# Performance work log

Measured on AMD Instinct MI355X. Metric: run time of the kernel, lower is better.

Reference implementation:

```python
import jax, jax.numpy as jnp
import numpy as np

B, NQ, NK, D, H = 4, 1025, 1024, 1024, 16
C = D // H          # per-head channels = 64
DFF = 1024          # FFN hidden, hard-coded in source
LN_EPS = 1e-5


def setup_inputs() -> dict:
    key = jax.random.key(0)
    ks = jax.random.split(key, 12)
    s = 0.02
    return {
        "q": jax.random.normal(ks[0], (B, NQ, D), jnp.float32),
        "k": jax.random.normal(ks[1], (B, NK, D), jnp.float32),
        "v": jax.random.normal(ks[2], (B, NK, D), jnp.float32),
        "w_qk": jax.random.normal(ks[3], (D, D), jnp.float32) * s,
        "dummy": jax.random.normal(ks[4], (1, D), jnp.float32),
        "w1": jax.random.normal(ks[5], (C, C // 2), jnp.float32) * s,
        "b1": jnp.zeros((C // 2,), jnp.float32),
        "w2": jax.random.normal(ks[6], (C, C // 2), jnp.float32) * s,
        "b2": jnp.zeros((C // 2,), jnp.float32),
        "w3": jax.random.normal(ks[7], (2 * C, C), jnp.float32) * s,
        "b3": jnp.zeros((C,), jnp.float32),
        "fw1": jax.random.normal(ks[8], (C, DFF), jnp.float32) * s,
        "fb1": jnp.zeros((DFF,), jnp.float32),
        "fw2": jax.random.normal(ks[9], (DFF, C), jnp.float32) * s,
        "fb2": jnp.zeros((C,), jnp.float32),
        "ln_g": jnp.ones((C,), jnp.float32),
        "ln_b": jnp.zeros((C,), jnp.float32),
    }


def _split_heads(x):
    # 'b n (h c) -> (b h) n c'
    b, n, _ = x.shape
    return x.reshape(b, n, H, C).transpose(0, 2, 1, 3).reshape(b * H, n, C)


def _l2norm(x):
    n = jnp.linalg.norm(x, axis=-1, keepdims=True)
    return x / jnp.maximum(n, 1e-12)


def reference(q, k, v, w_qk, dummy, w1, b1, w2, b2, w3, b3,
              fw1, fb1, fw2, fb2, ln_g, ln_b):
    b, nq, d = q.shape
    residual = q
    qp = q @ w_qk
    kp = jnp.concatenate(
        [k @ w_qk, jnp.broadcast_to(dummy[None], (b, 1, d))], axis=1)
    vp = jnp.concatenate([v, jnp.zeros((b, 1, d), v.dtype)], axis=1)

    qh, kh, vh, rh = map(_split_heads, (qp, kp, vp, residual))

    # cosine-similarity attention, ReLU instead of softmax (dropout p=0)
    attn = jnp.einsum('bic,bjc->bij', _l2norm(qh), _l2norm(kh))
    attn = jax.nn.relu(attn)
    out = jnp.einsum('bij,bjc->bic', attn, vh)  # (b*h, nq, c)

    o1 = jax.nn.relu((out * rh) @ w1 + b1)
    o2 = jax.nn.relu((rh - out) @ w2 + b2)
    o = jnp.concatenate([o1, o2, rh], axis=-1) @ w3 + b3

    # FFN with residual + LayerNorm (dropouts are identity at p=0)
    t = o + rh
    t = t + (jax.nn.relu(t @ fw1 + fb1) @ fw2 + fb2)
    mu = jnp.mean(t, axis=-1, keepdims=True)
    var = jnp.mean(jnp.square(t - mu), axis=-1, keepdims=True)
    t = (t - mu) / jnp.sqrt(var + LN_EPS) * ln_g + ln_b

    t = t + vh  # requires nq == nk + 1

    # '(b h) n c -> b n (h c)'
    return t.reshape(b, H, nq, C).transpose(0, 2, 1, 3).reshape(b, nq, d)
```

## Files before the change

kernel.cpp:

```cpp
#include <hip/hip_runtime.h>
#include <hip/hip_bf16.h>

#define DEV __device__ __forceinline__

typedef __attribute__((ext_vector_type(4))) float  f32x4;
typedef __attribute__((ext_vector_type(8))) short  s16x8;
typedef __attribute__((ext_vector_type(8))) __bf16 bf16x8;

#define NQ   1025
#define BH   64
#define NPAD 1152
#define MT   65600
#define DFF  1024

DEV short f2bf(float f){
  unsigned u = __builtin_bit_cast(unsigned, f);
  u = u + 0x7fffu + ((u >> 16) & 1u);
  return (short)(u >> 16);
}
DEV float bf2f(short s){
  unsigned u = ((unsigned)(unsigned short)s) << 16;
  return __builtin_bit_cast(float, u);
}
DEV f32x4 zero4(){ f32x4 z; z[0]=0.f; z[1]=0.f; z[2]=0.f; z[3]=0.f; return z; }
DEV s16x8 zero8(){ s16x8 z; for(int e=0;e<8;e++) z[e]=0; return z; }

DEV f32x4 mfma16(s16x8 a, s16x8 b, f32x4 c){
  return __builtin_amdgcn_mfma_f32_16x16x32_bf16(
      __builtin_bit_cast(bf16x8, a), __builtin_bit_cast(bf16x8, b), c, 0, 0, 0);
}

DEV void gll16(const void* g, void* l){
  __builtin_amdgcn_global_load_lds((const __attribute__((address_space(1))) void*)g,
                                   (__attribute__((address_space(3))) void*)l, 16, 0, 0);
}

DEV s16x8 lds_frag(const char* base, int row, int k8){
  int byte = row*128 + k8*2; byte ^= (row & 7) << 4;
  return *(const s16x8*)(base + byte);
}
DEV void lds_write16(char* base, int row, int k8, s16x8 v){
  int byte = row*128 + k8*2; byte ^= (row & 7) << 4;
  *(s16x8*)(base + byte) = v;
}
DEV void lds_write2(char* base, int row, int col, short v){
  int byte = row*128 + col*2; byte ^= (row & 7) << 4;
  *(short*)(base + byte) = v;
}
DEV void lds_w16_256(char* base, int row, int col, s16x8 v){
  int byte = row*256 + col*2; byte ^= (row & 7) << 4;
  *(s16x8*)(base + byte) = v;
}
DEV s16x8 lds_r16_256(const char* base, int row, int col){
  int byte = row*256 + col*2; byte ^= (row & 7) << 4;
  return *(const s16x8*)(base + byte);
}
DEV void lds_w2_256(char* base, int row, int col, short v){
  int byte = row*256 + col*2; byte ^= (row & 7) << 4;
  *(short*)(base + byte) = v;
}
DEV void blob_w16(char* blob, int row, int k8, s16x8 v){
  int byte = row*128 + k8*2; byte ^= (row & 7) << 4;
  *(s16x8*)(blob + byte) = v;
}

__global__ void k_tcvt(const float* __restrict__ in, int irs, int rin,
                       short* __restrict__ out, int ors){
  __shared__ float tile[32][33];
  int r0 = blockIdx.x*32, c0 = blockIdx.y*32;
  int tx = threadIdx.x, ty = threadIdx.y;
  for (int i=ty;i<32;i+=8){
    int r = r0+i;
    tile[i][tx] = (r < rin) ? in[(long)r*irs + c0 + tx] : 0.f;
  }
  __syncthreads();
  for (int i=ty;i<32;i+=8)
    out[(long)(c0+i)*ors + r0 + tx] = f2bf(tile[tx][i]);
}

__global__ __launch_bounds__(256)
void k_cvtA(const float* __restrict__ q, const float* __restrict__ kk, char* __restrict__ ab){
  int mt = blockIdx.x, kt = blockIdx.y;
  int tid = threadIdx.x;
  int r = tid>>1, ks = (tid&1)*32;
  int pr = mt*128 + r;
  int part = pr >= 4608;
  int pp = part ? pr-4608 : pr;
  int b = pp/NPAD, i = pp%NPAD;
  const float* src = nullptr;
  if (!part && i < 1025) src = q  + ((long)(b*1025+i))*1024 + kt*64 + ks;
  if ( part && i < 1024) src = kk + ((long)(b*1024+i))*1024 + kt*64 + ks;
  char* blob = ab + ((long)(mt*16+kt))*16384;
  #pragma unroll
  for (int c8=0;c8<32;c8+=8){
    s16x8 vv = zero8();
    if (src){
      f32x4 f0 = *(const f32x4*)(src + c8);
      f32x4 f1 = *(const f32x4*)(src + c8 + 4);
      #pragma unroll
      for(int e=0;e<4;e++){ vv[e]=f2bf(f0[e]); vv[4+e]=f2bf(f1[e]); }
    }
    blob_w16(blob, r, ks+c8, vv);
  }
}

__global__ __launch_bounds__(256)
void k_cvtW(const float* __restrict__ w, char* __restrict__ wb){
  __shared__ float T[64][129];
  int nt = blockIdx.x, kt = blockIdx.y;
  int tid = threadIdx.x;
  for (int idx=tid; idx<8192; idx+=256){
    int kr = idx>>7, nc = idx&127;
    T[kr][nc] = w[(long)(kt*64+kr)*1024 + nt*128+nc];
  }
  __syncthreads();
  int r = tid>>1, ks=(tid&1)*32;
  char* blob = wb + ((long)(nt*16+kt))*16384;
  #pragma unroll
  for (int c8=0;c8<32;c8+=8){
    s16x8 vv;
    #pragma unroll
    for(int e=0;e<8;e++) vv[e] = f2bf(T[ks+c8+e][r]);
    blob_w16(blob, r, ks+c8, vv);
  }
}

__global__ __launch_bounds__(256)
void k_cvtV(const float* __restrict__ v, char* __restrict__ vb){
  __shared__ float T[64][65];
  int jt = blockIdx.x, bh = blockIdx.y;
  int b = bh>>4, h = bh&15;
  int tid=threadIdx.x;
  for (int idx=tid; idx<4096; idx+=256){
    int jr = idx>>6, cc = idx&63;
    int j = jt*64+jr;
    T[jr][cc] = (j<1024)? v[((long)(b*1024+j))*1024 + h*64+cc] : 0.f;
  }
  __syncthreads();
  int r = tid>>2, js=(tid&3)*16;
  char* blob = vb + ((long)(bh*18+jt))*8192;
  #pragma unroll
  for (int c8=0;c8<16;c8+=8){
    s16x8 vv;
    #pragma unroll
    for(int e=0;e<8;e++) vv[e] = f2bf(T[js+c8+e][r]);
    blob_w16(blob, r, js+c8, vv);
  }
}

__global__ __launch_bounds__(256,2)
void k_proj(const char* __restrict__ ab, const char* __restrict__ wb,
            char* __restrict__ qpB, char* __restrict__ kpB,
            float* __restrict__ qnorm, float* __restrict__ knorm){
  __shared__ char SM[32768];
  char* A = SM; char* Bm = SM+16384;
  int flat = blockIdx.x;
  int g = (flat&7)*72 + (flat>>3);
  int mt = g>>3, nt = g&7;
  int tid=threadIdx.x, lane=tid&63, wv=tid>>6, lr=lane&15, lg=lane>>4;
  f32x4 acc[4][4];
  for(int a=0;a<4;a++) for(int b=0;b<4;b++) acc[a][b]=zero4();
  int wm=(wv>>1)*64, wn=(wv&1)*64;
  for (int kt=0; kt<16; kt++){
    const char* asrc = ab + ((long)(mt*16+kt))*16384 + wv*4096 + lane*16;
    const char* bsrc = wb + ((long)(nt*16+kt))*16384 + wv*4096 + lane*16;
    char* adst = A + wv*4096;  char* bdst = Bm + wv*4096;
    #pragma unroll
    for (int t=0;t<4;t++){
      gll16(asrc + t*1024, adst + t*1024);
      gll16(bsrc + t*1024, bdst + t*1024);
    }
    __syncthreads();
    #pragma unroll
    for (int kc=0;kc<64;kc+=32){
      int lk = kc + (lg<<3);
      s16x8 af[4], bfr[4];
      #pragma unroll
      for(int i=0;i<4;i++) af[i]  = lds_frag(A,  wm + i*16 + lr, lk);
      #pragma unroll
      for(int i=0;i<4;i++) bfr[i] = lds_frag(Bm, wn + i*16 + lr, lk);
      #pragma unroll
      for(int mi=0;mi<4;mi++)
        #pragma unroll
        for(int ni=0;ni<4;ni++) acc[mi][ni] = mfma16(af[mi], bfr[ni], acc[mi][ni]);
    }
    __syncthreads();
  }
  int head = nt*2 + (wv&1);
  #pragma unroll
  for(int mi=0;mi<4;mi++)
  #pragma unroll
  for(int j=0;j<4;j++){
    float ss = 0.f;
    #pragma unroll
    for(int ni=0;ni<4;ni++){ float x=acc[mi][ni][j]; ss += x*x; }
    ss += __shfl_xor(ss,1); ss += __shfl_xor(ss,2);
    ss += __shfl_xor(ss,4); ss += __shfl_xor(ss,8);
    if (lr==0){
      int pr = mt*128 + wm + mi*16 + lg*4 + j;
      int part = pr>=4608; int pp = part? pr-4608:pr;
      int b = pp/NPAD, i = pp%NPAD;
      float scv = 1.f/fmaxf(sqrtf(ss), 1e-12f);
      (part? knorm : qnorm)[(b*16+head)*NPAD + i] = scv;
    }
  }
  #pragma unroll
  for(int mi=0;mi<4;mi++)
  #pragma unroll
  for(int ni=0;ni<4;ni++)
  #pragma unroll
  for(int j=0;j<4;j++)
    lds_w2_256(SM, wm+mi*16+lg*4+j, wn+ni*16+lr, f2bf(acc[mi][ni][j]));
  __syncthreads();
  {
    int r = tid>>1, half = tid&1;
    int pr = mt*128 + r;
    int part = pr>=4608; int pp = part? pr-4608:pr;
    int b = pp/NPAD, i = pp%NPAD;
    int h2 = nt*2 + half;
    char* dst = (part? kpB : qpB) + ((long)((b*16+h2)*18 + (i>>6)))*8192;
    int rr = i&63;
    #pragma unroll
    for (int c8=0;c8<64;c8+=8){
      s16x8 vv = lds_r16_256(SM, r, half*64 + c8);
      blob_w16(dst, rr, c8, vv);
    }
  }
}

__global__ __launch_bounds__(256,2)
void k_attn(const char* __restrict__ qpB, const char* __restrict__ kpB,
            const char* __restrict__ vtB,
            const float* __restrict__ qnorm, const float* __restrict__ knorm,
            short* __restrict__ att){
  __shared__ char SM[49152];
  char* Q = SM; char* KT = SM+16384; char* VT = KT+8192; char* P = VT+8192;
  int flat = blockIdx.x;
  int g = (flat&7)*72 + (flat>>3);
  int bh = g/9, it = g%9;
  int i0 = it*128;
  int tid=threadIdx.x, lane=tid&63, wv=tid>>6, lr=lane&15, lg=lane>>4;
  {
    const char* src = qpB + ((long)(bh*18 + it*2))*8192 + wv*4096 + lane*16;
    char* dst = Q + wv*4096;
    #pragma unroll
    for (int t=0;t<4;t++) gll16(src + t*1024, dst + t*1024);
  }
  float rq[2][4];
  #pragma unroll
  for(int mi=0;mi<2;mi++)
  #pragma unroll
  for(int j=0;j<4;j++)
    rq[mi][j] = qnorm[bh*NPAD + i0 + wv*32+mi*16+lg*4+j];
  f32x4 oacc[2][4];
  for(int a=0;a<2;a++) for(int b=0;b<4;b++) oacc[a][b]=zero4();
  for (int jt=0; jt<18; ++jt){
    {
      const char* ks = kpB + ((long)(bh*18+jt))*8192 + wv*2048 + lane*16;
      const char* vs = vtB + ((long)(bh*18+jt))*8192 + wv*2048 + lane*16;
      gll16(ks,      KT + wv*2048);
      gll16(ks+1024, KT + wv*2048 + 1024);
      gll16(vs,      VT + wv*2048);
      gll16(vs+1024, VT + wv*2048 + 1024);
    }
    float rk[4];
    #pragma unroll
    for(int ni=0;ni<4;ni++) rk[ni] = knorm[bh*NPAD + jt*64 + ni*16+lr];
    __syncthreads();
    f32x4 sc[2][4];
    for(int a=0;a<2;a++) for(int b=0;b<4;b++) sc[a][b]=zero4();
    #pragma unroll
    for(int kc=0;kc<64;kc+=32){
      int lk = kc + (lg<<3);
      s16x8 af[2], bfr[4];
      #pragma unroll
      for(int i=0;i<2;i++) af[i]=lds_frag(Q, wv*32 + i*16 + lr, lk);
      #pragma unroll
      for(int i=0;i<4;i++) bfr[i]=lds_frag(KT, i*16 + lr, lk);
      #pragma unroll
      for(int mi=0;mi<2;mi++)
        #pragma unroll
        for(int ni=0;ni<4;ni++) sc[mi][ni]=mfma16(af[mi],bfr[ni],sc[mi][ni]);
    }
    #pragma unroll
    for(int mi=0;mi<2;mi++)
    #pragma unroll
    for(int ni=0;ni<4;ni++)
    #pragma unroll
    for(int j=0;j<4;j++){
      float x = sc[mi][ni][j] * rq[mi][j] * rk[ni];
      x = x>0.f?x:0.f;
      lds_write2(P, wv*32 + mi*16 + lg*4 + j, ni*16 + lr, f2bf(x));
    }
    __syncthreads();
    #pragma unroll
    for(int kc=0;kc<64;kc+=32){
      int lk = kc + (lg<<3);
      s16x8 pf[2], vf[4];
      #pragma unroll
      for(int i=0;i<2;i++) pf[i]=lds_frag(P, wv*32 + i*16 + lr, lk);
      #pragma unroll
      for(int i=0;i<4;i++) vf[i]=lds_frag(VT, i*16 + lr, lk);
      #pragma unroll
      for(int mi=0;mi<2;mi++)
        #pragma unroll
        for(int ni=0;ni<4;ni++) oacc[mi][ni]=mfma16(pf[mi],vf[ni],oacc[mi][ni]);
    }
    __syncthreads();
  }
  char* OS = SM+16384;
  #pragma unroll
  for(int mi=0;mi<2;mi++)
  #pragma unroll
  for(int ni=0;ni<4;ni++)
  #pragma unroll
  for(int j=0;j<4;j++)
    lds_write2(OS, wv*32+mi*16+lg*4+j, ni*16+lr, f2bf(oacc[mi][ni][j]));
  __syncthreads();
  {
    int r = tid>>1, half = tid&1;
    int i = i0 + r;
    if (i < 1025){
      short* dst = att + ((long)bh*1025 + i)*64 + half*32;
      #pragma unroll
      for (int u=0; u<32; u+=8){
        s16x8 vv = lds_frag(OS, r, half*32 + u);
        *(s16x8*)(dst + u) = vv;
      }
    }
  }
}

__global__ __launch_bounds__(256,1)
void k_tailpre(const short* __restrict__ att, const float* __restrict__ q,
    const float* __restrict__ w1, const float* __restrict__ b1,
    const float* __restrict__ w2, const float* __restrict__ b2,
    const float* __restrict__ w3, const float* __restrict__ b3,
    float* __restrict__ tf){
  __shared__ char X   [128*128*2];
  __shared__ char Y   [128*128*2];
  __shared__ char WbdT[ 64*128*2];
  __shared__ char W3T [ 64*128*2];
  long m0 = (long)blockIdx.x*128;
  int tid=threadIdx.x, lane=tid&63, wv=tid>>6, lr=lane&15, lg=lane>>4;
  for (int idx=tid; idx<64*128; idx+=256){
    int n = idx>>7, kx = idx&127;
    float wb = (n<32) ? (kx<64 ? w1[kx*32+n] : 0.f)
                      : (kx>=64 ? w2[(kx-64)*32+(n-32)] : 0.f);
    lds_w2_256(WbdT, n, kx, f2bf(wb));
    lds_w2_256(W3T,  n, kx, f2bf(w3[kx*64+n]));
  }
  {
    int r = tid>>1, ks=(tid&1)*32;
    long m = m0 + r;
    if (m < MT){
      int bh = (int)(m/1025); int i=(int)(m-(long)bh*1025); int b=bh>>4, h=bh&15;
      const short* asrc = att + m*64 + ks;
      const float* qsrc = q + ((long)b*1025 + i)*1024 + h*64 + ks;
      #pragma unroll
      for (int c8=0;c8<32;c8+=8){
        s16x8 av = *(const s16x8*)(asrc + c8);
        f32x4 q0 = *(const f32x4*)(qsrc + c8);
        f32x4 q1 = *(const f32x4*)(qsrc + c8 + 4);
        s16x8 x1v, x2v, rhv;
        #pragma unroll
        for(int e=0;e<4;e++){
          float o0=bf2f(av[e]),   r0=q0[e];
          float o1=bf2f(av[4+e]), r1=q1[e];
          x1v[e]=f2bf(o0*r0);   x1v[4+e]=f2bf(o1*r1);
          x2v[e]=f2bf(r0-o0);   x2v[4+e]=f2bf(r1-o1);
          rhv[e]=f2bf(r0);      rhv[4+e]=f2bf(r1);
        }
        lds_w16_256(X, r, ks+c8,    x1v);
        lds_w16_256(X, r, 64+ks+c8, x2v);
        lds_w16_256(Y, r, 64+ks+c8, rhv);
      }
    } else {
      s16x8 z = zero8();
      #pragma unroll
      for (int c8=0;c8<32;c8+=8){
        lds_w16_256(X, r, ks+c8, z);
        lds_w16_256(X, r, 64+ks+c8, z);
        lds_w16_256(Y, r, 64+ks+c8, z);
      }
    }
  }
  __syncthreads();
  f32x4 a1[2][4];
  for(int a=0;a<2;a++) for(int b=0;b<4;b++) a1[a][b]=zero4();
  #pragma unroll
  for (int kc=0;kc<128;kc+=32){
    int lk = kc + (lg<<3);
    s16x8 af[2], bfr[4];
    #pragma unroll
    for(int i=0;i<2;i++) af[i]=lds_r16_256(X, wv*32+i*16+lr, lk);
    #pragma unroll
    for(int i=0;i<4;i++) bfr[i]=lds_r16_256(WbdT, i*16+lr, lk);
    #pragma unroll
    for(int mi=0;mi<2;mi++)
      #pragma unroll
      for(int ni=0;ni<4;ni++) a1[mi][ni]=mfma16(af[mi],bfr[ni],a1[mi][ni]);
  }
  float bias12[4];
  #pragma unroll
  for(int ni=0;ni<4;ni++){ int cc=ni*16+lr; bias12[ni] = (cc<32)? b1[cc] : b2[cc-32]; }
  #pragma unroll
  for(int mi=0;mi<2;mi++)
  #pragma unroll
  for(int ni=0;ni<4;ni++)
  #pragma unroll
  for(int j=0;j<4;j++){
    int rr = wv*32+mi*16+lg*4+j;
    float x = a1[mi][ni][j] + bias12[ni];
    x = x>0.f?x:0.f;
    lds_w2_256(Y, rr, ni*16+lr, f2bf(x));
  }
  __syncthreads();
  f32x4 a2[2][4];
  for(int a=0;a<2;a++) for(int b=0;b<4;b++) a2[a][b]=zero4();
  #pragma unroll
  for (int kc=0;kc<128;kc+=32){
    int lk = kc + (lg<<3);
    s16x8 af[2], bfr[4];
    #pragma unroll
    for(int i=0;i<2;i++) af[i]=lds_r16_256(Y, wv*32+i*16+lr, lk);
    #pragma unroll
    for(int i=0;i<4;i++) bfr[i]=lds_r16_256(W3T, i*16+lr, lk);
    #pragma unroll
    for(int mi=0;mi<2;mi++)
      #pragma unroll
      for(int ni=0;ni<4;ni++) a2[mi][ni]=mfma16(af[mi],bfr[ni],a2[mi][ni]);
  }
  float b3v[4];
  #pragma unroll
  for(int ni=0;ni<4;ni++) b3v[ni] = b3[ni*16+lr];
  #pragma unroll
  for(int mi=0;mi<2;mi++)
  #pragma unroll
  for(int j=0;j<4;j++){
    long m = m0 + wv*32+mi*16+lg*4+j;
    if (m < MT){
      int bh = (int)(m/1025); int i=(int)(m-(long)bh*1025); int b=bh>>4, h=bh&15;
      const float* qsrc = q + ((long)b*1025 + i)*1024 + h*64;
      #pragma unroll
      for(int ni=0;ni<4;ni++){
        int cc = ni*16+lr;
        float rh = qsrc[cc];
        tf[m*64+cc] = a2[mi][ni][j] + b3v[ni] + rh;
      }
    }
  }
}

__global__ __launch_bounds__(256,2)
void k_ffn(const float* __restrict__ tf,
      const short* __restrict__ f1T, const short* __restrict__ f2T,
      const float* __restrict__ fb1, const float* __restrict__ fb2,
      const float* __restrict__ ln_g, const float* __restrict__ ln_b,
      const float* __restrict__ v, float* __restrict__ out){
  __shared__ char T [128*64*2];
  __shared__ char W1[ 64*64*2];
  __shared__ char U [128*64*2];
  __shared__ char W2[ 64*64*2];
  long m0 = (long)blockIdx.x*128;
  int tid=threadIdx.x, lane=tid&63, wv=tid>>6, lr=lane&15, lg=lane>>4;
  {
    int r=tid>>1, ks=(tid&1)*32; long m=m0+r;
    #pragma unroll
    for(int c8=0;c8<32;c8+=8){
      s16x8 vv = zero8();
      if (m<MT){
        f32x4 f0 = *(const f32x4*)(tf + m*64 + ks + c8);
        f32x4 f1 = *(const f32x4*)(tf + m*64 + ks + c8 + 4);
        #pragma unroll
        for(int e=0;e<4;e++){ vv[e]=f2bf(f0[e]); vv[4+e]=f2bf(f1[e]); }
      }
      lds_write16(T, r, ks+c8, vv);
    }
  }
  f32x4 acc2[2][4];
  for(int a=0;a<2;a++) for(int b=0;b<4;b++) acc2[a][b]=zero4();
  for (int d0=0; d0<DFF; d0+=64){
    {
      int r=tid>>2, ks=(tid&3)*16;
      const short* s1 = f1T + (long)(d0+r)*64 + ks;
      const short* s2 = f2T + (long)r*DFF + d0 + ks;
      #pragma unroll
      for(int c8=0;c8<16;c8+=8){
        lds_write16(W1, r, ks+c8, *(const s16x8*)(s1+c8));
        lds_write16(W2, r, ks+c8, *(const s16x8*)(s2+c8));
      }
    }
    __syncthreads();
    f32x4 sc[2][4];
    for(int a=0;a<2;a++) for(int b=0;b<4;b++) sc[a][b]=zero4();
    #pragma unroll
    for(int kc=0;kc<64;kc+=32){
      int lk = kc + (lg<<3);
      s16x8 af[2], bfr[4];
      #pragma unroll
      for(int i=0;i<2;i++) af[i]=lds_frag(T, wv*32+i*16+lr, lk);
      #pragma unroll
      for(int i=0;i<4;i++) bfr[i]=lds_frag(W1, i*16+lr, lk);
      #pragma unroll
      for(int mi=0;mi<2;mi++)
        #pragma unroll
        for(int ni=0;ni<4;ni++) sc[mi][ni]=mfma16(af[mi],bfr[ni],sc[mi][ni]);
    }
    #pragma unroll
    for(int mi=0;mi<2;mi++)
    #pragma unroll
    for(int ni=0;ni<4;ni++)
    #pragma unroll
    for(int j=0;j<4;j++){
      int uc = ni*16+lr;
      float x = sc[mi][ni][j] + fb1[d0+uc];
      x = x>0.f?x:0.f;
      lds_write2(U, wv*32+mi*16+lg*4+j, uc, f2bf(x));
    }
    __syncthreads();
    #pragma unroll
    for(int kc=0;kc<64;kc+=32){
      int lk = kc + (lg<<3);
      s16x8 uf[2], wf[4];
      #pragma unroll
      for(int i=0;i<2;i++) uf[i]=lds_frag(U, wv*32+i*16+lr, lk);
      #pragma unroll
      for(int i=0;i<4;i++) wf[i]=lds_frag(W2, i*16+lr, lk);
      #pragma unroll
      for(int mi=0;mi<2;mi++)
        #pragma unroll
        for(int ni=0;ni<4;ni++) acc2[mi][ni]=mfma16(uf[mi],wf[ni],acc2[mi][ni]);
    }
    __syncthreads();
  }
  #pragma unroll
  for(int mi=0;mi<2;mi++){
    float xv[4][4];
    long mbase = m0 + wv*32 + mi*16 + lg*4;
    #pragma unroll
    for(int ni=0;ni<4;ni++)
    #pragma unroll
    for(int j=0;j<4;j++){
      long m = mbase + j;
      int c = ni*16+lr;
      float t = (m<MT)? tf[m*64+c] : 0.f;
      xv[ni][j] = acc2[mi][ni][j] + fb2[c] + t;
    }
    #pragma unroll
    for(int j=0;j<4;j++){
      float s = xv[0][j]+xv[1][j]+xv[2][j]+xv[3][j];
      #pragma unroll
      for(int mm=1;mm<16;mm<<=1) s += __shfl_xor(s, mm);
      float mu = s*(1.f/64.f);
      float vs = 0.f;
      #pragma unroll
      for(int ni=0;ni<4;ni++){ float d2=xv[ni][j]-mu; vs += d2*d2; }
      #pragma unroll
      for(int mm=1;mm<16;mm<<=1) vs += __shfl_xor(vs, mm);
      float inv = rsqrtf(vs*(1.f/64.f) + 1e-5f);
      long m = mbase + j;
      if (m < MT){
        int bh = (int)(m/1025); int i = (int)(m - (long)bh*1025);
        int b = bh>>4, h = bh&15;
        #pragma unroll
        for(int ni=0;ni<4;ni++){
          int c = ni*16+lr;
          float y = (xv[ni][j]-mu)*inv*ln_g[c] + ln_b[c];
          float vh = (i<1024)? v[((long)b*1024 + i)*1024 + h*64 + c] : 0.f;
          out[((long)b*1025 + i)*1024 + h*64 + c] = y + vh;
        }
      }
    }
  }
}

extern "C" void kernel_launch(void* const* d_in, const int* in_sizes, int n_in,
                              void* d_out, int out_size, void* d_ws, size_t ws_size,
                              hipStream_t stream) {
  const float* q    = (const float*)d_in[0];
  const float* k    = (const float*)d_in[1];
  const float* v    = (const float*)d_in[2];
  const float* w_qk = (const float*)d_in[3];
  const float* w1   = (const float*)d_in[5];
  const float* b1   = (const float*)d_in[6];
  const float* w2   = (const float*)d_in[7];
  const float* b2   = (const float*)d_in[8];
  const float* w3   = (const float*)d_in[9];
  const float* b3   = (const float*)d_in[10];
  const float* fw1  = (const float*)d_in[11];
  const float* fb1  = (const float*)d_in[12];
  const float* fw2  = (const float*)d_in[13];
  const float* fb2  = (const float*)d_in[14];
  const float* ln_g = (const float*)d_in[15];
  const float* ln_b = (const float*)d_in[16];
  float* out = (float*)d_out;

  char* ws = (char*)d_ws;
  const size_t OFF_A   = 0;
  const size_t SZ_A    = 25190400;
  const size_t OFF_WB  = OFF_A + SZ_A;
  const size_t OFF_F1T = OFF_WB  + (size_t)8*16*16384;
  const size_t OFF_F2T = OFF_F1T + (size_t)1024*64*2;
  const size_t OFF_VT  = OFF_F2T + (size_t)64*1024*2;
  const size_t OFF_QP  = OFF_VT  + (size_t)64*18*8192;
  const size_t OFF_KP  = OFF_QP  + (size_t)64*18*8192;
  const size_t OFF_QN  = OFF_KP  + (size_t)64*18*8192;
  const size_t OFF_KN  = OFF_QN  + (size_t)BH*NPAD*4;
  const size_t NEEDED  = OFF_KN  + (size_t)BH*NPAD*4;
  if (ws_size < NEEDED) return;

  char*  ab   = ws + OFF_A;
  short* att  = (short*)(ws + OFF_A);
  float* tf   = (float*)(ws + OFF_A + 8396800);
  char*  wb   = ws + OFF_WB;
  short* f1T  = (short*)(ws + OFF_F1T);
  short* f2T  = (short*)(ws + OFF_F2T);
  char*  vtB  = ws + OFF_VT;
  char*  qpB  = ws + OFF_QP;
  char*  kpB  = ws + OFF_KP;
  float* qnorm= (float*)(ws + OFF_QN);
  float* knorm= (float*)(ws + OFF_KN);

  k_cvtA<<<dim3(72,16), 256, 0, stream>>>(q, k, ab);
  k_cvtW<<<dim3(8,16),  256, 0, stream>>>(w_qk, wb);
  k_cvtV<<<dim3(18,64), 256, 0, stream>>>(v, vtB);
  k_tcvt<<<dim3(2,32),  dim3(32,8), 0, stream>>>(fw1, 1024, 64,  f1T, 64);
  k_tcvt<<<dim3(32,2),  dim3(32,8), 0, stream>>>(fw2, 64,  1024, f2T, 1024);
  k_proj<<<576, 256, 0, stream>>>(ab, wb, qpB, kpB, qnorm, knorm);
  k_attn<<<576, 256, 0, stream>>>(qpB, kpB, vtB, qnorm, knorm, att);
  k_tailpre<<<513, 256, 0, stream>>>(att, q, w1, b1, w2, b2, w3, b3, tf);
  k_ffn<<<513, 256, 0, stream>>>(tf, f1T, f2T, fb1, fb2, ln_g, ln_b, v, out);
}
```

Measured before the change: 209.0 us.

## Fuse tail projection and FFN kernels with double-buffered async weight loads

Merges k_tailpre and k_ffn into one k_tail kernel, so the fp32 intermediate tf no longer makes a round trip through global memory, and one launch is dropped. The block-diagonal w1/w2 GEMM is split into two dense 64-wide halves, which skips the zero-padded multiplies. The w3 GEMM is split over the out and residual halves. FFN weight tiles are now prefetched with direct global-to-LDS loads into a double buffer, which removes one barrier per iteration. LDS grows to 80KB per block while the launch bound asks for 2 blocks, and some barriers are removed, so the ordering of reuse of R1/R3 within a wave has to stay correct.

```diff
diff --git a/kernel.cpp b/kernel.cpp
--- a/kernel.cpp
+++ b/kernel.cpp
@@ -331,38 +331,44 @@
   }
 }
 
-__global__ __launch_bounds__(256,1)
-void k_tailpre(const short* __restrict__ att, const float* __restrict__ q,
+__global__ __launch_bounds__(256,2)
+void k_tail(const short* __restrict__ att, const float* __restrict__ q,
     const float* __restrict__ w1, const float* __restrict__ b1,
     const float* __restrict__ w2, const float* __restrict__ b2,
     const float* __restrict__ w3, const float* __restrict__ b3,
-    float* __restrict__ tf){
-  __shared__ char X   [128*128*2];
-  __shared__ char Y   [128*128*2];
-  __shared__ char WbdT[ 64*128*2];
-  __shared__ char W3T [ 64*128*2];
+    const short* __restrict__ f1T, const short* __restrict__ f2T,
+    const float* __restrict__ fb1, const float* __restrict__ fb2,
+    const float* __restrict__ ln_g, const float* __restrict__ ln_b,
+    const float* __restrict__ v, float* __restrict__ out){
+  __shared__ char SM[81920];
+  char* R1 = SM;
+  char* R2 = SM + 16384;
+  char* R3 = SM + 32768;
+  char* WP = SM + 49152;
   long m0 = (long)blockIdx.x*128;
   int tid=threadIdx.x, lane=tid&63, wv=tid>>6, lr=lane&15, lg=lane>>4;
-  for (int idx=tid; idx<64*128; idx+=256){
-    int n = idx>>7, kx = idx&127;
-    float wb = (n<32) ? (kx<64 ? w1[kx*32+n] : 0.f)
-                      : (kx>=64 ? w2[(kx-64)*32+(n-32)] : 0.f);
-    lds_w2_256(WbdT, n, kx, f2bf(wb));
-    lds_w2_256(W3T,  n, kx, f2bf(w3[kx*64+n]));
+  for (int idx=tid; idx<2048; idx+=256){
+    int n=idx>>6, c=idx&63;
+    lds_write2(WP,      n, c, f2bf(w1[c*32+n]));
+    lds_write2(WP+4096, n, c, f2bf(w2[c*32+n]));
+  }
+  for (int idx=tid; idx<8192; idx+=256){
+    int n=idx>>7, kx=idx&127;
+    lds_w2_256(WP+8192, n, kx, f2bf(w3[kx*64+n]));
   }
   {
     int r = tid>>1, ks=(tid&1)*32;
     long m = m0 + r;
     if (m < MT){
-      int bh = (int)(m/1025); int i=(int)(m-(long)bh*1025); int b=bh>>4, h=bh&15;
+      int bh=(int)(m/1025); int i=(int)(m-(long)bh*1025); int b=bh>>4, h=bh&15;
       const short* asrc = att + m*64 + ks;
-      const float* qsrc = q + ((long)b*1025 + i)*1024 + h*64 + ks;
+      const float* qsrc = q + ((long)b*1025+i)*1024 + h*64 + ks;
       #pragma unroll
       for (int c8=0;c8<32;c8+=8){
         s16x8 av = *(const s16x8*)(asrc + c8);
         f32x4 q0 = *(const f32x4*)(qsrc + c8);
         f32x4 q1 = *(const f32x4*)(qsrc + c8 + 4);
-        s16x8 x1v, x2v, rhv;
+        s16x8 x1v,x2v,rhv;
         #pragma unroll
         for(int e=0;e<4;e++){
           float o0=bf2f(av[e]),   r0=q0[e];
@@ -371,17 +377,17 @@
           x2v[e]=f2bf(r0-o0);   x2v[4+e]=f2bf(r1-o1);
           rhv[e]=f2bf(r0);      rhv[4+e]=f2bf(r1);
         }
-        lds_w16_256(X, r, ks+c8,    x1v);
-        lds_w16_256(X, r, 64+ks+c8, x2v);
-        lds_w16_256(Y, r, 64+ks+c8, rhv);
+        lds_write16(R1, r, ks+c8, x1v);
+        lds_write16(R2, r, ks+c8, x2v);
+        lds_write16(R3, r, ks+c8, rhv);
       }
     } else {
       s16x8 z = zero8();
       #pragma unroll
       for (int c8=0;c8<32;c8+=8){
-        lds_w16_256(X, r, ks+c8, z);
-        lds_w16_256(X, r, 64+ks+c8, z);
-        lds_w16_256(Y, r, 64+ks+c8, z);
+        lds_write16(R1, r, ks+c8, z);
+        lds_write16(R2, r, ks+c8, z);
+        lds_write16(R3, r, ks+c8, z);
       }
     }
   }
@@ -389,17 +395,24 @@
   f32x4 a1[2][4];
   for(int a=0;a<2;a++) for(int b=0;b<4;b++) a1[a][b]=zero4();
   #pragma unroll
-  for (int kc=0;kc<128;kc+=32){
+  for (int kc=0;kc<64;kc+=32){
     int lk = kc + (lg<<3);
-    s16x8 af[2], bfr[4];
-    #pragma unroll
-    for(int i=0;i<2;i++) af[i]=lds_r16_256(X, wv*32+i*16+lr, lk);
-    #pragma unroll
-    for(int i=0;i<4;i++) bfr[i]=lds_r16_256(WbdT, i*16+lr, lk);
-    #pragma unroll
-    for(int mi=0;mi<2;mi++)
-      #pragma unroll
-      for(int ni=0;ni<4;ni++) a1[mi][ni]=mfma16(af[mi],bfr[ni],a1[mi][ni]);
+    s16x8 af1[2], af2[2], bw1[2], bw2[2];
+    #pragma unroll
+    for(int i=0;i<2;i++){
+      af1[i]=lds_frag(R1, wv*32+i*16+lr, lk);
+      af2[i]=lds_frag(R2, wv*32+i*16+lr, lk);
+      bw1[i]=lds_frag(WP,      i*16+lr, lk);
+      bw2[i]=lds_frag(WP+4096, i*16+lr, lk);
+    }
+    #pragma unroll
+    for(int mi=0;mi<2;mi++){
+      #pragma unroll
+      for(int ni=0;ni<2;ni++){
+        a1[mi][ni]   = mfma16(af1[mi], bw1[ni], a1[mi][ni]);
+        a1[mi][2+ni] = mfma16(af2[mi], bw2[ni], a1[mi][2+ni]);
+      }
+    }
   }
   float bias12[4];
   #pragma unroll
@@ -410,88 +423,90 @@
   for(int ni=0;ni<4;ni++)
   #pragma unroll
   for(int j=0;j<4;j++){
-    int rr = wv*32+mi*16+lg*4+j;
     float x = a1[mi][ni][j] + bias12[ni];
     x = x>0.f?x:0.f;
-    lds_w2_256(Y, rr, ni*16+lr, f2bf(x));
-  }
-  __syncthreads();
+    lds_write2(R1, wv*32+mi*16+lg*4+j, ni*16+lr, f2bf(x));
+  }
   f32x4 a2[2][4];
   for(int a=0;a<2;a++) for(int b=0;b<4;b++) a2[a][b]=zero4();
   #pragma unroll
-  for (int kc=0;kc<128;kc+=32){
+  for (int kc=0;kc<64;kc+=32){
     int lk = kc + (lg<<3);
-    s16x8 af[2], bfr[4];
-    #pragma unroll
-    for(int i=0;i<2;i++) af[i]=lds_r16_256(Y, wv*32+i*16+lr, lk);
-    #pragma unroll
-    for(int i=0;i<4;i++) bfr[i]=lds_r16_256(W3T, i*16+lr, lk);
+    s16x8 ao[2], ar[2], bo[4], br[4];
+    #pragma unroll
+    for(int i=0;i<2;i++){
+      ao[i]=lds_frag(R1, wv*32+i*16+lr, lk);
+      ar[i]=lds_frag(R3, wv*32+i*16+lr, lk);
+    }
+    #pragma unroll
+    for(int i=0;i<4;i++){
+      bo[i]=lds_r16_256(WP+8192, i*16+lr, lk);
+      br[i]=lds_r16_256(WP+8192, i*16+lr, 64+lk);
+    }
     #pragma unroll
     for(int mi=0;mi<2;mi++)
       #pragma unroll
-      for(int ni=0;ni<4;ni++) a2[mi][ni]=mfma16(af[mi],bfr[ni],a2[mi][ni]);
-  }
-  float b3v[4];
-  #pragma unroll
-  for(int ni=0;ni<4;ni++) b3v[ni] = b3[ni*16+lr];
-  #pragma unroll
-  for(int mi=0;mi<2;mi++)
-  #pragma unroll
-  for(int j=0;j<4;j++){
-    long m = m0 + wv*32+mi*16+lg*4+j;
-    if (m < MT){
-      int bh = (int)(m/1025); int i=(int)(m-(long)bh*1025); int b=bh>>4, h=bh&15;
-      const float* qsrc = q + ((long)b*1025 + i)*1024 + h*64;
+      for(int ni=0;ni<4;ni++){
+        a2[mi][ni]=mfma16(ao[mi],bo[ni],a2[mi][ni]);
+        a2[mi][ni]=mfma16(ar[mi],br[ni],a2[mi][ni]);
+      }
+  }
+  float tv[2][4][4];
+  {
+    float b3v[4];
+    #pragma unroll
+    for(int ni=0;ni<4;ni++) b3v[ni] = b3[ni*16+lr];
+    #pragma unroll
+    for(int mi=0;mi<2;mi++)
+    #pragma unroll
+    for(int j=0;j<4;j++){
+      long m = m0 + wv*32+mi*16+lg*4+j;
+      int bh=0,i=0,b=0,h=0; const float* qsrc = nullptr;
+      if (m < MT){ bh=(int)(m/1025); i=(int)(m-(long)bh*1025); b=bh>>4; h=bh&15;
+                   qsrc = q + ((long)b*1025+i)*1024 + h*64; }
       #pragma unroll
       for(int ni=0;ni<4;ni++){
         int cc = ni*16+lr;
-        float rh = qsrc[cc];
-        tf[m*64+cc] = a2[mi][ni][j] + b3v[ni] + rh;
-      }
-    }
-  }
-}
-
-__global__ __launch_bounds__(256,2)
-void k_ffn(const float* __restrict__ tf,
-      const short* __restrict__ f1T, const short* __restrict__ f2T,
-      const float* __restrict__ fb1, const float* __restrict__ fb2,
-      const float* __restrict__ ln_g, const float* __restrict__ ln_b,
-      const float* __restrict__ v, float* __restrict__ out){
-  __shared__ char T [128*64*2];
-  __shared__ char W1[ 64*64*2];
-  __shared__ char U [128*64*2];
-  __shared__ char W2[ 64*64*2];
-  long m0 = (long)blockIdx.x*128;
-  int tid=threadIdx.x, lane=tid&63, wv=tid>>6, lr=lane&15, lg=lane>>4;
+        float rh = qsrc ? qsrc[cc] : 0.f;
+        float t = a2[mi][ni][j] + b3v[ni] + rh;
+        tv[mi][ni][j] = t;
+        lds_write2(R2, wv*32+mi*16+lg*4+j, cc, f2bf(t));
+      }
+    }
+  }
+  __syncthreads();
   {
-    int r=tid>>1, ks=(tid&1)*32; long m=m0+r;
-    #pragma unroll
-    for(int c8=0;c8<32;c8+=8){
-      s16x8 vv = zero8();
-      if (m<MT){
-        f32x4 f0 = *(const f32x4*)(tf + m*64 + ks + c8);
-        f32x4 f1 = *(const f32x4*)(tf + m*64 + ks + c8 + 4);
-        #pragma unroll
-        for(int e=0;e<4;e++){ vv[e]=f2bf(f0[e]); vv[4+e]=f2bf(f1[e]); }
-      }
-      lds_write16(T, r, ks+c8, vv);
-    }
-  }
+    const char* f1 = (const char*)f1T;
+    const char* f2 = (const char*)f2T;
+    #pragma unroll
+    for (int t=0;t<2;t++){
+      int seg = wv + t*4;
+      int o = seg*1024 + lane*16;
+      int r = o>>7, wb = o&127;
+      int swb = wb ^ ((r&7)<<4);
+      gll16(f1 + r*128 + swb,        WP + o);
+      gll16(f2 + (long)r*2048 + swb, WP + 16384 + o);
+    }
+  }
+  __syncthreads();
   f32x4 acc2[2][4];
   for(int a=0;a<2;a++) for(int b=0;b<4;b++) acc2[a][b]=zero4();
-  for (int d0=0; d0<DFF; d0+=64){
-    {
-      int r=tid>>2, ks=(tid&3)*16;
-      const short* s1 = f1T + (long)(d0+r)*64 + ks;
-      const short* s2 = f2T + (long)r*DFF + d0 + ks;
-      #pragma unroll
-      for(int c8=0;c8<16;c8+=8){
-        lds_write16(W1, r, ks+c8, *(const s16x8*)(s1+c8));
-        lds_write16(W2, r, ks+c8, *(const s16x8*)(s2+c8));
-      }
-    }
-    __syncthreads();
+  int p = 0;
+  for (int d=0; d<16; ++d){
+    if (d < 15){
+      const char* f1 = (const char*)f1T;
+      const char* f2 = (const char*)f2T;
+      int dn = d+1, pn = p^1;
+      #pragma unroll
+      for (int t=0;t<2;t++){
+        int seg = wv + t*4;
+        int o = seg*1024 + lane*16;
+        int r = o>>7, wb = o&127;
+        int swb = wb ^ ((r&7)<<4);
+        gll16(f1 + (long)dn*8192 + r*128 + swb, WP + pn*8192 + o);
+        gll16(f2 + (long)r*2048 + dn*128 + swb, WP + 16384 + pn*8192 + o);
+      }
+    }
     f32x4 sc[2][4];
     for(int a=0;a<2;a++) for(int b=0;b<4;b++) sc[a][b]=zero4();
     #pragma unroll
@@ -499,9 +514,9 @@
       int lk = kc + (lg<<3);
       s16x8 af[2], bfr[4];
       #pragma unroll
-      for(int i=0;i<2;i++) af[i]=lds_frag(T, wv*32+i*16+lr, lk);
-      #pragma unroll
-      for(int i=0;i<4;i++) bfr[i]=lds_frag(W1, i*16+lr, lk);
+      for(int i=0;i<2;i++) af[i]=lds_frag(R2, wv*32+i*16+lr, lk);
+      #pragma unroll
+      for(int i=0;i<4;i++) bfr[i]=lds_frag(WP + p*8192, i*16+lr, lk);
       #pragma unroll
       for(int mi=0;mi<2;mi++)
         #pragma unroll
@@ -514,25 +529,25 @@
     #pragma unroll
     for(int j=0;j<4;j++){
       int uc = ni*16+lr;
-      float x = sc[mi][ni][j] + fb1[d0+uc];
+      float x = sc[mi][ni][j] + fb1[d*64+uc];
       x = x>0.f?x:0.f;
-      lds_write2(U, wv*32+mi*16+lg*4+j, uc, f2bf(x));
-    }
-    __syncthreads();
+      lds_write2(R3, wv*32+mi*16+lg*4+j, uc, f2bf(x));
+    }
     #pragma unroll
     for(int kc=0;kc<64;kc+=32){
       int lk = kc + (lg<<3);
       s16x8 uf[2], wf[4];
       #pragma unroll
-      for(int i=0;i<2;i++) uf[i]=lds_frag(U, wv*32+i*16+lr, lk);
-      #pragma unroll
-      for(int i=0;i<4;i++) wf[i]=lds_frag(W2, i*16+lr, lk);
+      for(int i=0;i<2;i++) uf[i]=lds_frag(R3, wv*32+i*16+lr, lk);
+      #pragma unroll
+      for(int i=0;i<4;i++) wf[i]=lds_frag(WP + 16384 + p*8192, i*16+lr, lk);
       #pragma unroll
       for(int mi=0;mi<2;mi++)
         #pragma unroll
         for(int ni=0;ni<4;ni++) acc2[mi][ni]=mfma16(uf[mi],wf[ni],acc2[mi][ni]);
     }
     __syncthreads();
+    p ^= 1;
   }
   #pragma unroll
   for(int mi=0;mi<2;mi++){
@@ -542,10 +557,8 @@
     for(int ni=0;ni<4;ni++)
     #pragma unroll
     for(int j=0;j<4;j++){
-      long m = mbase + j;
       int c = ni*16+lr;
-      float t = (m<MT)? tf[m*64+c] : 0.f;
-      xv[ni][j] = acc2[mi][ni][j] + fb2[c] + t;
+      xv[ni][j] = acc2[mi][ni][j] + fb2[c] + tv[mi][ni][j];
     }
     #pragma unroll
     for(int j=0;j<4;j++){
@@ -612,7 +625,6 @@
 
   char*  ab   = ws + OFF_A;
   short* att  = (short*)(ws + OFF_A);
-  float* tf   = (float*)(ws + OFF_A + 8396800);
   char*  wb   = ws + OFF_WB;
   short* f1T  = (short*)(ws + OFF_F1T);
   short* f2T  = (short*)(ws + OFF_F2T);
@@ -629,6 +641,6 @@
   k_tcvt<<<dim3(32,2),  dim3(32,8), 0, stream>>>(fw2, 64,  1024, f2T, 1024);
   k_proj<<<576, 256, 0, stream>>>(ab, wb, qpB, kpB, qnorm, knorm);
   k_attn<<<576, 256, 0, stream>>>(qpB, kpB, vtB, qnorm, knorm, att);
-  k_tailpre<<<513, 256, 0, stream>>>(att, q, w1, b1, w2, b2, w3, b3, tf);
-  k_ffn<<<513, 256, 0, stream>>>(tf, f1T, f2T, fb1, fb2, ln_g, ln_b, v, out);
-}
+  k_tail<<<513, 256, 0, stream>>>(att, q, w1, b1, w2, b2, w3, b3,
+                                  f1T, f2T, fb1, fb2, ln_g, ln_b, v, out);
+}
```

Result: slower. 214.6 us (+2.7%).
